# Kernel tuning notes

Measured on AMD Instinct MI355X. Metric: run time of the kernel, lower is better.

The kernel has to match this reference:

```python
import jax, jax.numpy as jnp
import numpy as np

N, S, Z, H, K, DEG = 8192, 4, 64, 128, 4, 16
E = N * DEG


def setup_inputs() -> dict:
    key = jax.random.key(0)
    ks = jax.random.split(key, 9)
    g = lambda k, shape, scale=1.0: jax.random.normal(k, shape, dtype=jnp.float32) * scale
    return dict(
        zIG=g(ks[0], (N, S, Z)),                         # node intention features
        xt_enc=g(ks[1], (N, S, H)),                      # encoded actions per node
        Ws=g(ks[2], (K, H, Z), 1.0 / np.sqrt(Z)),        # attn_s[k] weights (no bias)
        Wd=g(ks[3], (K, H, Z), 1.0 / np.sqrt(Z)),        # attn_d[k] weights
        F2_w1=g(ks[4], (H, 2 * H), 1.0 / np.sqrt(2 * H)),
        F2_w2=g(ks[5], (H, H), 1.0 / np.sqrt(H)),
        F1_w1=g(ks[6], (H, K * H), 1.0 / np.sqrt(K * H)),
        F1_w2=g(ks[7], (H, H), 1.0 / np.sqrt(H)),
        src=jax.random.randint(ks[8], (E,), 0, N),       # random source per edge
        dst=jnp.repeat(jnp.arange(N), DEG),              # regular graph: DEG in-edges per node, grouped
    )


def reference(zIG, xt_enc, Ws, Wd, F2_w1, F2_w2, F1_w1, F1_w2, src, dst):
    n, s, h = xt_enc.shape
    k = Ws.shape[0]
    deg = src.shape[0] // n

    # ---- edge_attention: eIG[e,s,k] = leaky_relu(sum_h (Ws_k z_src)*(Wd_k z_dst)) ----
    zs, zd = zIG[src], zIG[dst]                          # [E,S,Z] irregular gathers
    scores = []
    for kk in range(k):                                  # k is small & structural
        a_s = zs @ Ws[kk].T                              # [E,S,H]
        a_d = zd @ Wd[kk].T                              # [E,S,H]
        scores.append(jax.nn.leaky_relu((a_s * a_d).sum(-1)))  # [E,S]
    eIG = jnp.stack(scores, axis=-1)                     # [E,S,K]

    # ---- message_func: dA = F2(cat(xt_src, xt_dst)) ----
    msg_in = jnp.concatenate([xt_enc[src], xt_enc[dst]], axis=-1)   # [E,S,2H]
    dA = jax.nn.relu(msg_in @ F2_w1.T) @ F2_w2.T                    # [E,S,H]

    # ---- reduce_func: softmax over neighbor mailbox (dim=1), weighted mean ----
    # dst is grouped with constant degree, so the DGL mailbox is a reshape.
    alpha = jax.nn.softmax(eIG.reshape(n, deg, s, k), axis=1)       # [N,D,S,K]
    mail = dA.reshape(n, deg, s, h)                                 # [N,D,S,H]
    res = jnp.einsum('ndsk,ndsh->nskh', alpha, mail) / deg          # mean over D
    res = res.reshape(n, s, k * h)                                  # cat over k (k-major)
    deltax = jax.nn.relu(res @ F1_w1.T) @ F1_w2.T                   # [N,S,H]
    return deltax, alpha
```

## Files before the change

kernel.cpp:

```cpp
#include <hip/hip_runtime.h>
#include <hip/hip_bf16.h>

typedef unsigned short u16;
typedef unsigned int u32;
using ushort8 = __attribute__((ext_vector_type(8))) unsigned short;
using short8  = __attribute__((ext_vector_type(8))) short;
using f32x4   = __attribute__((ext_vector_type(4))) float;

__device__ __forceinline__ float bf2f(u16 v) {
  union { u32 u; float f; } x; x.u = ((u32)v) << 16; return x.f;
}
__device__ __forceinline__ float u2f(u32 u) {
  union { u32 u; float f; } x; x.u = u; return x.f;
}
__device__ __forceinline__ u16 f2bf(float f) {
  union { u32 u; float f; } x; x.f = f;
  u32 r = x.u + 0x7FFFu + ((x.u >> 16) & 1u);
  return (u16)(r >> 16);
}
__device__ __forceinline__ u32 pack2bf(float lo, float hi) {
  return (u32)f2bf(lo) | ((u32)f2bf(hi) << 16);
}
__device__ __forceinline__ float dot4(float4 a, float4 b) {
  return a.x * b.x + a.y * b.y + a.z * b.z + a.w * b.w;
}
__device__ __forceinline__ void split8(const float* ap, short8& hi, short8& lo) {
  float4 a0 = *(const float4*)ap, a1 = *(const float4*)(ap + 4);
  float e[8] = {a0.x, a0.y, a0.z, a0.w, a1.x, a1.y, a1.z, a1.w};
  u16 h[8], l[8];
  #pragma unroll
  for (int j = 0; j < 8; ++j) {
    u32 b = __float_as_uint(e[j]);
    h[j] = (u16)(b >> 16);
    l[j] = f2bf(e[j] - u2f(b & 0xffff0000u));
  }
  hi = *(short8*)h; lo = *(short8*)l;
}
__device__ __forceinline__ void stage_w(const float* g, int stride, int c, u16* Wl, int t) {
  int row = t >> 1, half = t & 1;
  const float4* gp = (const float4*)(g + (size_t)row * stride + c * 64 + half * 32);
  ushort8* d = (ushort8*)(Wl + row * 72 + half * 32);
  #pragma unroll
  for (int i = 0; i < 4; ++i) {
    float4 a = gp[2 * i], b = gp[2 * i + 1];
    ushort8 o;
    o[0] = f2bf(a.x); o[1] = f2bf(a.y); o[2] = f2bf(a.z); o[3] = f2bf(a.w);
    o[4] = f2bf(b.x); o[5] = f2bf(b.y); o[6] = f2bf(b.z); o[7] = f2bf(b.w);
    d[i] = o;
  }
}
__device__ __forceinline__ void stage_w512(const float* g, int stride, int c, u16* Wl, int t) {
  int row = t >> 2, q = t & 3;
  const float4* gp = (const float4*)(g + (size_t)row * stride + c * 64 + q * 16);
  ushort8* d = (ushort8*)(Wl + row * 72 + q * 16);
  #pragma unroll
  for (int i = 0; i < 2; ++i) {
    float4 a = gp[2 * i], b = gp[2 * i + 1];
    ushort8 o;
    o[0] = f2bf(a.x); o[1] = f2bf(a.y); o[2] = f2bf(a.z); o[3] = f2bf(a.w);
    o[4] = f2bf(b.x); o[5] = f2bf(b.y); o[6] = f2bf(b.z); o[7] = f2bf(b.w);
    d[i] = o;
  }
}

__global__ __launch_bounds__(256) void k_prep(const float* __restrict__ Ws,
                                              const float* __restrict__ Wd,
                                              const float* __restrict__ F1w1,
                                              const float* __restrict__ F2w2,
                                              u16* __restrict__ Bh, u16* __restrict__ Bl,
                                              float* __restrict__ WW2) {
  if (blockIdx.x < 64) {
    int t = blockIdx.x * 256 + threadIdx.x;
    int k = t >> 12, z1 = (t >> 6) & 63, z2 = t & 63;
    const float* wsp = Ws + k * 8192 + z1;
    const float* wdp = Wd + k * 8192 + z2;
    float acc = 0.f;
    #pragma unroll 8
    for (int h = 0; h < 128; ++h) acc += wsp[h * 64] * wdp[h * 64];
    u32 b = __float_as_uint(acc);
    Bh[(k * 64 + z1) * 64 + z2] = (u16)(b >> 16);
    Bl[(k * 64 + z1) * 64 + z2] = f2bf(acc - u2f(b & 0xffff0000u));
  } else {
    int id = (blockIdx.x - 64) * 256 + threadIdx.x;
    int ho = id >> 9, kk = (id >> 7) & 3, hi = id & 127;
    const float* wa = F1w1 + ho * 512 + kk * 128;
    const float* wb = F2w2 + hi;
    float acc = 0.f;
    #pragma unroll 8
    for (int j = 0; j < 128; ++j) acc += wa[j] * wb[j * 128];
    WW2[ho * 512 + kk * 128 + hi] = acc * 0.0625f;
  }
}

__global__ __launch_bounds__(256) void k_tduv(const float* __restrict__ zIG,
                                              const u16* __restrict__ Bh_g,
                                              const u16* __restrict__ Bl_g,
                                              const float* __restrict__ xt,
                                              const float* __restrict__ W1,
                                              float* __restrict__ td,
                                              u16* __restrict__ u, u16* __restrict__ v) {
  __shared__ __align__(16) u16 SM[128 * 72];
  int t = threadIdx.x, lane = t & 63, w = t >> 6;
  int l15 = lane & 15, kc = lane >> 4;
  if (blockIdx.x < 1024) {
    u16* Bh = SM;
    u16* Bl = SM + 64 * 72;
    int cq = blockIdx.x & 3;
    size_t rowbase = (size_t)(blockIdx.x >> 2) * 128 + w * 32;
    {
      int row = t >> 2, q = t & 3;
      const ushort8* gh = (const ushort8*)(Bh_g + (cq * 64 + row) * 64 + q * 16);
      const ushort8* gl = (const ushort8*)(Bl_g + (cq * 64 + row) * 64 + q * 16);
      ushort8* dh = (ushort8*)(Bh + row * 72 + q * 16);
      ushort8* dl = (ushort8*)(Bl + row * 72 + q * 16);
      dh[0] = gh[0]; dh[1] = gh[1];
      dl[0] = gl[0]; dl[1] = gl[1];
    }
    __syncthreads();
    f32x4 acc[2][4];
    #pragma unroll
    for (int mt = 0; mt < 2; ++mt)
      #pragma unroll
      for (int nt = 0; nt < 4; ++nt) acc[mt][nt] = (f32x4){0.f, 0.f, 0.f, 0.f};
    #pragma unroll
    for (int ks = 0; ks < 2; ++ks) {
      short8 ah[2], al[2];
      #pragma unroll
      for (int mt = 0; mt < 2; ++mt)
        split8(zIG + (rowbase + mt * 16 + l15) * 64 + ks * 32 + kc * 8, ah[mt], al[mt]);
      #pragma unroll
      for (int nt = 0; nt < 4; ++nt) {
        int bo = (nt * 16 + l15) * 72 + ks * 32 + kc * 8;
        short8 bh = *(const short8*)&Bh[bo];
        short8 bl = *(const short8*)&Bl[bo];
        #pragma unroll
        for (int mt = 0; mt < 2; ++mt) {
          acc[mt][nt] = __builtin_amdgcn_mfma_f32_16x16x32_bf16(ah[mt], bh, acc[mt][nt], 0, 0, 0);
          acc[mt][nt] = __builtin_amdgcn_mfma_f32_16x16x32_bf16(al[mt], bh, acc[mt][nt], 0, 0, 0);
          acc[mt][nt] = __builtin_amdgcn_mfma_f32_16x16x32_bf16(ah[mt], bl, acc[mt][nt], 0, 0, 0);
        }
      }
    }
    #pragma unroll
    for (int mt = 0; mt < 2; ++mt)
      #pragma unroll
      for (int nt = 0; nt < 4; ++nt)
        #pragma unroll
        for (int j = 0; j < 4; ++j)
          td[(rowbase + mt * 16 + kc * 4 + j) * 256 + cq * 64 + nt * 16 + l15] =
              acc[mt][nt][j];
  } else {
    u16* Wl = SM;
    int bid2 = blockIdx.x - 1024;
    int sel = bid2 >> 8;
    size_t rowbase = (size_t)(bid2 & 255) * 128 + w * 32;
    const float* Wbase = W1 + sel * 128;
    f32x4 acc[2][8];
    #pragma unroll
    for (int mt = 0; mt < 2; ++mt)
      #pragma unroll
      for (int nt = 0; nt < 8; ++nt) acc[mt][nt] = (f32x4){0.f, 0.f, 0.f, 0.f};
    for (int c = 0; c < 2; ++c) {
      __syncthreads();
      stage_w(Wbase, 256, c, Wl, t);
      __syncthreads();
      #pragma unroll
      for (int ks = 0; ks < 2; ++ks) {
        short8 af[2];
        #pragma unroll
        for (int mt = 0; mt < 2; ++mt) {
          const float* ap = xt + (rowbase + mt * 16 + l15) * 128 + c * 64 + ks * 32 + kc * 8;
          float4 a0 = *(const float4*)ap, a1 = *(const float4*)(ap + 4);
          u16 tmp[8] = {f2bf(a0.x), f2bf(a0.y), f2bf(a0.z), f2bf(a0.w),
                        f2bf(a1.x), f2bf(a1.y), f2bf(a1.z), f2bf(a1.w)};
          af[mt] = *(short8*)tmp;
        }
        #pragma unroll
        for (int nt = 0; nt < 8; ++nt) {
          short8 bw = *(const short8*)&Wl[(nt * 16 + l15) * 72 + ks * 32 + kc * 8];
          #pragma unroll
          for (int mt = 0; mt < 2; ++mt)
            acc[mt][nt] = __builtin_amdgcn_mfma_f32_16x16x32_bf16(af[mt], bw, acc[mt][nt], 0, 0, 0);
        }
      }
    }
    u16* dstp = sel ? v : u;
    #pragma unroll
    for (int mt = 0; mt < 2; ++mt)
      #pragma unroll
      for (int nt = 0; nt < 8; ++nt)
        #pragma unroll
        for (int j = 0; j < 4; ++j)
          dstp[(rowbase + mt * 16 + kc * 4 + j) * 128 + nt * 16 + l15] =
              f2bf(acc[mt][nt][j]);
  }
}

__global__ __launch_bounds__(256) void k_score(
    const float* __restrict__ zIG, const int* __restrict__ src,
    const float* __restrict__ td, const u16* __restrict__ uW, const u16* __restrict__ vW,
    float* __restrict__ out, u16* __restrict__ m_ws) {
  __shared__ int srcIdx[16];
  __shared__ float tds[16 * 68];
  __shared__ float s17[16 * 17];
  __shared__ float a20[16 * 20];

  int t = threadIdx.x, n = blockIdx.x;
  if (t < 16) srcIdx[t] = src[n * 16 + t];
  {
    int r = t >> 4, cc = t & 15;
    *(float4*)&tds[r * 68 + cc * 4] = ((const float4*)(td + (size_t)n * 1024))[r * 16 + cc];
  }
  __syncthreads();
  int hp = t & 63, sD = t >> 6;
  const u32* up = (const u32*)uW;
  u32 upre[16];
  #pragma unroll
  for (int dd = 0; dd < 16; ++dd)
    upre[dd] = up[(size_t)srcIdx[dd] * 256 + sD * 64 + hp];
  u32 vbits = *(const u32*)(vW + (size_t)n * 512 + sD * 128 + hp * 2);
  {
    int d = t >> 4, s = (t >> 2) & 3, k = t & 3;
    int sn = srcIdx[d];
    const float4* zp = (const float4*)(zIG + (size_t)sn * 256 + s * 64);
    int base = s * 4;
    float p0 = 0.f, p1 = 0.f, p2 = 0.f, p3 = 0.f;
    #pragma unroll
    for (int i = 0; i < 4; ++i) {
      float4 zv = zp[i * 4 + k];
      int o = i * 16 + k * 4;
      p0 += dot4(zv, *(const float4*)&tds[(base + 0) * 68 + o]);
      p1 += dot4(zv, *(const float4*)&tds[(base + 1) * 68 + o]);
      p2 += dot4(zv, *(const float4*)&tds[(base + 2) * 68 + o]);
      p3 += dot4(zv, *(const float4*)&tds[(base + 3) * 68 + o]);
    }
    p0 += __shfl_xor(p0, 1); p1 += __shfl_xor(p1, 1);
    p2 += __shfl_xor(p2, 1); p3 += __shfl_xor(p3, 1);
    p0 += __shfl_xor(p0, 2); p1 += __shfl_xor(p1, 2);
    p2 += __shfl_xor(p2, 2); p3 += __shfl_xor(p3, 2);
    float acc = (k == 0) ? p0 : (k == 1) ? p1 : (k == 2) ? p2 : p3;
    s17[d * 17 + base + k] = acc > 0.f ? acc : 0.01f * acc;
  }
  __syncthreads();
  {
    int d = t >> 4, sk = t & 15;
    float mx = -3.4e38f;
    #pragma unroll
    for (int dd = 0; dd < 16; ++dd) mx = fmaxf(mx, s17[dd * 17 + sk]);
    float sum = 0.f, eown = 0.f;
    #pragma unroll
    for (int dd = 0; dd < 16; ++dd) {
      float e = __expf(s17[dd * 17 + sk] - mx);
      sum += e;
      if (dd == d) eown = e;
    }
    float a = eown / sum;
    a20[d * 20 + sk] = a;
    out[4194304u + (unsigned)n * 256 + t] = a;
  }
  __syncthreads();
  {
    float v_lo = u2f(vbits << 16), v_hi = u2f(vbits & 0xffff0000u);
    float m0l = 0.f, m0h = 0.f, m1l = 0.f, m1h = 0.f;
    float m2l = 0.f, m2h = 0.f, m3l = 0.f, m3h = 0.f;
    #pragma unroll
    for (int dd = 0; dd < 16; ++dd) {
      u32 ub = upre[dd];
      float r_lo = fmaxf(u2f(ub << 16) + v_lo, 0.f);
      float r_hi = fmaxf(u2f(ub & 0xffff0000u) + v_hi, 0.f);
      float4 a = *(const float4*)&a20[dd * 20 + sD * 4];
      m0l += a.x * r_lo; m0h += a.x * r_hi;
      m1l += a.y * r_lo; m1h += a.y * r_hi;
      m2l += a.z * r_lo; m2h += a.z * r_hi;
      m3l += a.w * r_lo; m3h += a.w * r_hi;
    }
    u32* mp = (u32*)(m_ws + (size_t)n * 2048);
    mp[(sD * 4 + 0) * 64 + hp] = pack2bf(m0l, m0h);
    mp[(sD * 4 + 1) * 64 + hp] = pack2bf(m1l, m1h);
    mp[(sD * 4 + 2) * 64 + hp] = pack2bf(m2l, m2h);
    mp[(sD * 4 + 3) * 64 + hp] = pack2bf(m3l, m3h);
  }
}

__global__ __launch_bounds__(512) void k_fg(const u16* __restrict__ A,
                                            const float* __restrict__ WF,
                                            const float* __restrict__ WG,
                                            float* __restrict__ out) {
  __shared__ u16 Wl[128 * 72];
  __shared__ u16 hidl[128 * 136];
  int t = threadIdx.x, lane = t & 63, w = t >> 6;
  size_t rowbase = (size_t)blockIdx.x * 128 + w * 16;
  int l15 = lane & 15, kc = lane >> 4;
  f32x4 acc[8];
  #pragma unroll
  for (int nt = 0; nt < 8; ++nt) acc[nt] = (f32x4){0.f, 0.f, 0.f, 0.f};
  for (int c = 0; c < 8; ++c) {
    __syncthreads();
    stage_w512(WF, 512, c, Wl, t);
    __syncthreads();
    #pragma unroll
    for (int ks = 0; ks < 2; ++ks) {
      short8 af = *(const short8*)(A + (rowbase + l15) * 512 + c * 64 + ks * 32 + kc * 8);
      #pragma unroll
      for (int nt = 0; nt < 8; ++nt) {
        short8 bf = *(const short8*)&Wl[(nt * 16 + l15) * 72 + ks * 32 + kc * 8];
        acc[nt] = __builtin_amdgcn_mfma_f32_16x16x32_bf16(af, bf, acc[nt], 0, 0, 0);
      }
    }
  }
  #pragma unroll
  for (int nt = 0; nt < 8; ++nt)
    #pragma unroll
    for (int j = 0; j < 4; ++j)
      hidl[(w * 16 + kc * 4 + j) * 136 + nt * 16 + l15] = f2bf(fmaxf(acc[nt][j], 0.f));
  f32x4 acc2[8];
  #pragma unroll
  for (int nt = 0; nt < 8; ++nt) acc2[nt] = (f32x4){0.f, 0.f, 0.f, 0.f};
  for (int c = 0; c < 2; ++c) {
    __syncthreads();
    stage_w512(WG, 128, c, Wl, t);
    __syncthreads();
    #pragma unroll
    for (int ks = 0; ks < 2; ++ks) {
      short8 af = *(const short8*)&hidl[(w * 16 + l15) * 136 + c * 64 + ks * 32 + kc * 8];
      #pragma unroll
      for (int nt = 0; nt < 8; ++nt) {
        short8 bf = *(const short8*)&Wl[(nt * 16 + l15) * 72 + ks * 32 + kc * 8];
        acc2[nt] = __builtin_amdgcn_mfma_f32_16x16x32_bf16(af, bf, acc2[nt], 0, 0, 0);
      }
    }
  }
  #pragma unroll
  for (int nt = 0; nt < 8; ++nt)
    #pragma unroll
    for (int j = 0; j < 4; ++j)
      out[(rowbase + kc * 4 + j) * 128 + nt * 16 + l15] = acc2[nt][j];
}

extern "C" void kernel_launch(void* const* d_in, const int* in_sizes, int n_in,
                              void* d_out, int out_size, void* d_ws, size_t ws_size,
                              hipStream_t stream) {
  const float* zIG  = (const float*)d_in[0];
  const float* xt   = (const float*)d_in[1];
  const float* Ws   = (const float*)d_in[2];
  const float* Wd   = (const float*)d_in[3];
  const float* F2w1 = (const float*)d_in[4];
  const float* F2w2 = (const float*)d_in[5];
  const float* F1w1 = (const float*)d_in[6];
  const float* F1w2 = (const float*)d_in[7];
  const int* src    = (const int*)d_in[8];
  float* out = (float*)d_out;

  char* ws = (char*)d_ws;
  u16* Bh    = (u16*)ws;
  u16* Bl    = Bh + 16384;
  float* td  = (float*)(ws + 65536);
  u16* u     = (u16*)(ws + 65536 + 33554432);
  u16* v     = u + 4194304;
  float* WW2 = (float*)(ws + 50397184);
  u16* m     = (u16*)(ws + 50659328);

  k_prep <<<320,  256, 0, stream>>>(Ws, Wd, F1w1, F2w2, Bh, Bl, WW2);
  k_tduv <<<1536, 256, 0, stream>>>(zIG, Bh, Bl, xt, F2w1, td, u, v);
  k_score<<<8192, 256, 0, stream>>>(zIG, src, td, u, v, out, m);
  k_fg   <<<256,  512, 0, stream>>>(m, WW2, F1w2, out);
}
```

Measured before the change: 100.7 us.

## Compute edge scores with split-bf16 MFMA, one node per wavefront

The per-edge attention score dot products in k_score move from scalar fp32 dot4 loops to split hi/lo bf16 MFMA instructions, using a new pre-split bf16 copy of zIG made in k_prep and td stored as hi/lo bf16 pairs. Each wavefront now handles one node, so the softmax runs with shuffles and two block barriers are dropped. The goal is to cut VALU work and shared-memory staging in the score kernel. The cost is an extra conversion pass over zIG and additional workspace, and split-bf16 accuracy is slightly below fp32.

Measured after the change: 100.9 us. No clear change (+0.1%).

```diff
diff --git a/kernel.cpp b/kernel.cpp
--- a/kernel.cpp
+++ b/kernel.cpp
@@ -3,6 +3,7 @@
 
 typedef unsigned short u16;
 typedef unsigned int u32;
+typedef unsigned long long u64;
 using ushort8 = __attribute__((ext_vector_type(8))) unsigned short;
 using short8  = __attribute__((ext_vector_type(8))) short;
 using f32x4   = __attribute__((ext_vector_type(4))) float;
@@ -20,9 +21,6 @@
 }
 __device__ __forceinline__ u32 pack2bf(float lo, float hi) {
   return (u32)f2bf(lo) | ((u32)f2bf(hi) << 16);
-}
-__device__ __forceinline__ float dot4(float4 a, float4 b) {
-  return a.x * b.x + a.y * b.y + a.z * b.z + a.w * b.w;
 }
 __device__ __forceinline__ void split8(const float* ap, short8& hi, short8& lo) {
   float4 a0 = *(const float4*)ap, a1 = *(const float4*)(ap + 4);
@@ -67,8 +65,10 @@
                                               const float* __restrict__ Wd,
                                               const float* __restrict__ F1w1,
                                               const float* __restrict__ F2w2,
+                                              const float* __restrict__ zIG,
                                               u16* __restrict__ Bh, u16* __restrict__ Bl,
-                                              float* __restrict__ WW2) {
+                                              float* __restrict__ WW2,
+                                              u16* __restrict__ zh, u16* __restrict__ zl) {
   if (blockIdx.x < 64) {
     int t = blockIdx.x * 256 + threadIdx.x;
     int k = t >> 12, z1 = (t >> 6) & 63, z2 = t & 63;
@@ -80,7 +80,7 @@
     u32 b = __float_as_uint(acc);
     Bh[(k * 64 + z1) * 64 + z2] = (u16)(b >> 16);
     Bl[(k * 64 + z1) * 64 + z2] = f2bf(acc - u2f(b & 0xffff0000u));
-  } else {
+  } else if (blockIdx.x < 320) {
     int id = (blockIdx.x - 64) * 256 + threadIdx.x;
     int ho = id >> 9, kk = (id >> 7) & 3, hi = id & 127;
     const float* wa = F1w1 + ho * 512 + kk * 128;
@@ -89,6 +89,23 @@
     #pragma unroll 8
     for (int j = 0; j < 128; ++j) acc += wa[j] * wb[j * 128];
     WW2[ho * 512 + kk * 128 + hi] = acc * 0.0625f;
+  } else {
+    int base = (blockIdx.x - 320) * 256 + threadIdx.x;
+    #pragma unroll
+    for (int i = 0; i < 16; ++i) {
+      int idx = base + i * 32768;
+      float4 zv = ((const float4*)zIG)[idx];
+      float e[4] = {zv.x, zv.y, zv.z, zv.w};
+      u16 h[4], l[4];
+      #pragma unroll
+      for (int j = 0; j < 4; ++j) {
+        u32 b = __float_as_uint(e[j]);
+        h[j] = (u16)(b >> 16);
+        l[j] = f2bf(e[j] - u2f(b & 0xffff0000u));
+      }
+      *(u64*)&zh[idx * 4] = *(u64*)h;
+      *(u64*)&zl[idx * 4] = *(u64*)l;
+    }
   }
 }
 
@@ -97,7 +114,7 @@
                                               const u16* __restrict__ Bl_g,
                                               const float* __restrict__ xt,
                                               const float* __restrict__ W1,
-                                              float* __restrict__ td,
+                                              u16* __restrict__ tdh, u16* __restrict__ tdl,
                                               u16* __restrict__ u, u16* __restrict__ v) {
   __shared__ __align__(16) u16 SM[128 * 72];
   int t = threadIdx.x, lane = t & 63, w = t >> 6;
@@ -146,9 +163,13 @@
       #pragma unroll
       for (int nt = 0; nt < 4; ++nt)
         #pragma unroll
-        for (int j = 0; j < 4; ++j)
-          td[(rowbase + mt * 16 + kc * 4 + j) * 256 + cq * 64 + nt * 16 + l15] =
-              acc[mt][nt][j];
+        for (int j = 0; j < 4; ++j) {
+          float val = acc[mt][nt][j];
+          size_t idx = (rowbase + mt * 16 + kc * 4 + j) * 256 + cq * 64 + nt * 16 + l15;
+          u32 b = __float_as_uint(val);
+          tdh[idx] = (u16)(b >> 16);
+          tdl[idx] = f2bf(val - u2f(b & 0xffff0000u));
+        }
   } else {
     u16* Wl = SM;
     int bid2 = blockIdx.x - 1024;
@@ -197,88 +218,97 @@
 }
 
 __global__ __launch_bounds__(256) void k_score(
-    const float* __restrict__ zIG, const int* __restrict__ src,
-    const float* __restrict__ td, const u16* __restrict__ uW, const u16* __restrict__ vW,
+    const u16* __restrict__ zh, const u16* __restrict__ zl,
+    const u16* __restrict__ tdh, const u16* __restrict__ tdl,
+    const int* __restrict__ src, const u16* __restrict__ uW, const u16* __restrict__ vW,
     float* __restrict__ out, u16* __restrict__ m_ws) {
-  __shared__ int srcIdx[16];
-  __shared__ float tds[16 * 68];
-  __shared__ float s17[16 * 17];
-  __shared__ float a20[16 * 20];
-
-  int t = threadIdx.x, n = blockIdx.x;
-  if (t < 16) srcIdx[t] = src[n * 16 + t];
+  __shared__ float a20[4][320];
+
+  int t = threadIdx.x, lane = t & 63, w = t >> 6;
+  int n = blockIdx.x * 4 + w;
+  int l15 = lane & 15, lq = lane >> 4;
+
+  const u16* tdh_n = tdh + (size_t)n * 1024;
+  const u16* tdl_n = tdl + (size_t)n * 1024;
+  short8 bh0 = *(const short8*)(tdh_n + l15 * 64 + lq * 8);
+  short8 bh1 = *(const short8*)(tdh_n + l15 * 64 + 32 + lq * 8);
+  short8 bl0 = *(const short8*)(tdl_n + l15 * 64 + lq * 8);
+  short8 bl1 = *(const short8*)(tdl_n + l15 * 64 + 32 + lq * 8);
+  size_t zrow = (size_t)src[n * 16 + l15] * 256;
+  f32x4 acc[4];
+  #pragma unroll
+  for (int s = 0; s < 4; ++s) {
+    short8 ah0 = *(const short8*)(zh + zrow + s * 64 + lq * 8);
+    short8 ah1 = *(const short8*)(zh + zrow + s * 64 + 32 + lq * 8);
+    short8 al0 = *(const short8*)(zl + zrow + s * 64 + lq * 8);
+    short8 al1 = *(const short8*)(zl + zrow + s * 64 + 32 + lq * 8);
+    f32x4 a = (f32x4){0.f, 0.f, 0.f, 0.f};
+    a = __builtin_amdgcn_mfma_f32_16x16x32_bf16(ah0, bh0, a, 0, 0, 0);
+    a = __builtin_amdgcn_mfma_f32_16x16x32_bf16(ah1, bh1, a, 0, 0, 0);
+    a = __builtin_amdgcn_mfma_f32_16x16x32_bf16(al0, bh0, a, 0, 0, 0);
+    a = __builtin_amdgcn_mfma_f32_16x16x32_bf16(al1, bh1, a, 0, 0, 0);
+    a = __builtin_amdgcn_mfma_f32_16x16x32_bf16(ah0, bl0, a, 0, 0, 0);
+    a = __builtin_amdgcn_mfma_f32_16x16x32_bf16(ah1, bl1, a, 0, 0, 0);
+    acc[s] = a;
+  }
+  int qsel = l15 >> 2;
+  float sc[4];
+  #pragma unroll
+  for (int j = 0; j < 4; ++j) {
+    float a01 = (qsel == 0) ? acc[0][j] : acc[1][j];
+    float a23 = (qsel == 2) ? acc[2][j] : acc[3][j];
+    float vsc = (qsel < 2) ? a01 : a23;
+    sc[j] = vsc > 0.f ? vsc : 0.01f * vsc;
+  }
+  float mx = fmaxf(fmaxf(sc[0], sc[1]), fmaxf(sc[2], sc[3]));
+  mx = fmaxf(mx, __shfl_xor(mx, 16));
+  mx = fmaxf(mx, __shfl_xor(mx, 32));
+  float e0 = __expf(sc[0] - mx), e1 = __expf(sc[1] - mx);
+  float e2 = __expf(sc[2] - mx), e3 = __expf(sc[3] - mx);
+  float esum = (e0 + e1) + (e2 + e3);
+  esum += __shfl_xor(esum, 16);
+  esum += __shfl_xor(esum, 32);
+  float inv = 1.0f / esum;
+  float al[4] = {e0 * inv, e1 * inv, e2 * inv, e3 * inv};
   {
-    int r = t >> 4, cc = t & 15;
-    *(float4*)&tds[r * 68 + cc * 4] = ((const float4*)(td + (size_t)n * 1024))[r * 16 + cc];
+    float* ob = out + 4194304u + (unsigned)n * 256;
+    #pragma unroll
+    for (int j = 0; j < 4; ++j) {
+      int d = lq * 4 + j;
+      ob[d * 16 + l15] = al[j];
+      a20[w][d * 20 + l15] = al[j];
+    }
   }
   __syncthreads();
-  int hp = t & 63, sD = t >> 6;
+  int sidx[16];
+  #pragma unroll
+  for (int dd = 0; dd < 16; ++dd) sidx[dd] = src[n * 16 + dd];
   const u32* up = (const u32*)uW;
-  u32 upre[16];
-  #pragma unroll
-  for (int dd = 0; dd < 16; ++dd)
-    upre[dd] = up[(size_t)srcIdx[dd] * 256 + sD * 64 + hp];
-  u32 vbits = *(const u32*)(vW + (size_t)n * 512 + sD * 128 + hp * 2);
-  {
-    int d = t >> 4, s = (t >> 2) & 3, k = t & 3;
-    int sn = srcIdx[d];
-    const float4* zp = (const float4*)(zIG + (size_t)sn * 256 + s * 64);
-    int base = s * 4;
-    float p0 = 0.f, p1 = 0.f, p2 = 0.f, p3 = 0.f;
-    #pragma unroll
-    for (int i = 0; i < 4; ++i) {
-      float4 zv = zp[i * 4 + k];
-      int o = i * 16 + k * 4;
-      p0 += dot4(zv, *(const float4*)&tds[(base + 0) * 68 + o]);
-      p1 += dot4(zv, *(const float4*)&tds[(base + 1) * 68 + o]);
-      p2 += dot4(zv, *(const float4*)&tds[(base + 2) * 68 + o]);
-      p3 += dot4(zv, *(const float4*)&tds[(base + 3) * 68 + o]);
-    }
-    p0 += __shfl_xor(p0, 1); p1 += __shfl_xor(p1, 1);
-    p2 += __shfl_xor(p2, 1); p3 += __shfl_xor(p3, 1);
-    p0 += __shfl_xor(p0, 2); p1 += __shfl_xor(p1, 2);
-    p2 += __shfl_xor(p2, 2); p3 += __shfl_xor(p3, 2);
-    float acc = (k == 0) ? p0 : (k == 1) ? p1 : (k == 2) ? p2 : p3;
-    s17[d * 17 + base + k] = acc > 0.f ? acc : 0.01f * acc;
-  }
-  __syncthreads();
-  {
-    int d = t >> 4, sk = t & 15;
-    float mx = -3.4e38f;
-    #pragma unroll
-    for (int dd = 0; dd < 16; ++dd) mx = fmaxf(mx, s17[dd * 17 + sk]);
-    float sum = 0.f, eown = 0.f;
-    #pragma unroll
-    for (int dd = 0; dd < 16; ++dd) {
-      float e = __expf(s17[dd * 17 + sk] - mx);
-      sum += e;
-      if (dd == d) eown = e;
-    }
-    float a = eown / sum;
-    a20[d * 20 + sk] = a;
-    out[4194304u + (unsigned)n * 256 + t] = a;
-  }
-  __syncthreads();
-  {
-    float v_lo = u2f(vbits << 16), v_hi = u2f(vbits & 0xffff0000u);
+  u32* mp = (u32*)(m_ws + (size_t)n * 2048);
+  #pragma unroll
+  for (int s = 0; s < 4; ++s) {
+    u32 vb = *(const u32*)(vW + (size_t)n * 512 + s * 128 + lane * 2);
+    float v_lo = u2f(vb << 16), v_hi = u2f(vb & 0xffff0000u);
+    u32 ub[16];
+    #pragma unroll
+    for (int dd = 0; dd < 16; ++dd)
+      ub[dd] = up[(size_t)sidx[dd] * 256 + s * 64 + lane];
     float m0l = 0.f, m0h = 0.f, m1l = 0.f, m1h = 0.f;
     float m2l = 0.f, m2h = 0.f, m3l = 0.f, m3h = 0.f;
     #pragma unroll
     for (int dd = 0; dd < 16; ++dd) {
-      u32 ub = upre[dd];
-      float r_lo = fmaxf(u2f(ub << 16) + v_lo, 0.f);
-      float r_hi = fmaxf(u2f(ub & 0xffff0000u) + v_hi, 0.f);
-      float4 a = *(const float4*)&a20[dd * 20 + sD * 4];
+      float r_lo = fmaxf(u2f(ub[dd] << 16) + v_lo, 0.f);
+      float r_hi = fmaxf(u2f(ub[dd] & 0xffff0000u) + v_hi, 0.f);
+      float4 a = *(const float4*)&a20[w][dd * 20 + s * 4];
       m0l += a.x * r_lo; m0h += a.x * r_hi;
       m1l += a.y * r_lo; m1h += a.y * r_hi;
       m2l += a.z * r_lo; m2h += a.z * r_hi;
       m3l += a.w * r_lo; m3h += a.w * r_hi;
     }
-    u32* mp = (u32*)(m_ws + (size_t)n * 2048);
-    mp[(sD * 4 + 0) * 64 + hp] = pack2bf(m0l, m0h);
-    mp[(sD * 4 + 1) * 64 + hp] = pack2bf(m1l, m1h);
-    mp[(sD * 4 + 2) * 64 + hp] = pack2bf(m2l, m2h);
-    mp[(sD * 4 + 3) * 64 + hp] = pack2bf(m3l, m3h);
+    mp[(s * 4 + 0) * 64 + lane] = pack2bf(m0l, m0h);
+    mp[(s * 4 + 1) * 64 + lane] = pack2bf(m1l, m1h);
+    mp[(s * 4 + 2) * 64 + lane] = pack2bf(m2l, m2h);
+    mp[(s * 4 + 3) * 64 + lane] = pack2bf(m3l, m3h);
   }
 }
 
@@ -353,15 +383,18 @@
 
   char* ws = (char*)d_ws;
   u16* Bh    = (u16*)ws;
-  u16* Bl    = Bh + 16384;
-  float* td  = (float*)(ws + 65536);
-  u16* u     = (u16*)(ws + 65536 + 33554432);
-  u16* v     = u + 4194304;
-  float* WW2 = (float*)(ws + 50397184);
-  u16* m     = (u16*)(ws + 50659328);
-
-  k_prep <<<320,  256, 0, stream>>>(Ws, Wd, F1w1, F2w2, Bh, Bl, WW2);
-  k_tduv <<<1536, 256, 0, stream>>>(zIG, Bh, Bl, xt, F2w1, td, u, v);
-  k_score<<<8192, 256, 0, stream>>>(zIG, src, td, u, v, out, m);
+  u16* Bl    = (u16*)(ws + 32768);
+  u16* tdh   = (u16*)(ws + 65536);
+  u16* tdl   = (u16*)(ws + 16842752);
+  u16* u     = (u16*)(ws + 33619968);
+  u16* v     = (u16*)(ws + 42008576);
+  u16* zh    = (u16*)(ws + 50397184);
+  u16* zl    = (u16*)(ws + 54591488);
+  float* WW2 = (float*)(ws + 58785792);
+  u16* m     = (u16*)(ws + 59047936);
+
+  k_prep <<<448,  256, 0, stream>>>(Ws, Wd, F1w1, F2w2, zIG, Bh, Bl, WW2, zh, zl);
+  k_tduv <<<1536, 256, 0, stream>>>(zIG, Bh, Bl, xt, F2w1, tdh, tdl, u, v);
+  k_score<<<2048, 256, 0, stream>>>(zh, zl, tdh, tdl, src, u, v, out, m);
   k_fg   <<<256,  512, 0, stream>>>(m, WW2, F1w2, out);
 }
```
